# Performance work log

Measured on AMD Instinct MI355X. Metric: run time of the kernel, lower is better.

Reference implementation:

```python
import jax, jax.numpy as jnp
import numpy as np

DIM = 128
NUM_HEADS = 8


def setup_inputs() -> dict:
    key = jax.random.key(0)
    ks = jax.random.split(key, 5)
    B, L, C = 4, 16384, DIM
    x = jax.random.normal(ks[0], (B, L, C), dtype=jnp.float32)
    # Linear params (stored as (in, out) so y = x @ W + b)
    w_qkv = jax.random.normal(ks[1], (C, 3 * C), dtype=jnp.float32) * (C ** -0.5)
    b_qkv = jax.random.normal(ks[2], (3 * C,), dtype=jnp.float32) * 0.02
    w_proj = jax.random.normal(ks[3], (C, C), dtype=jnp.float32) * (C ** -0.5)
    b_proj = jax.random.normal(ks[4], (C,), dtype=jnp.float32) * 0.02
    return {"x": x, "w_qkv": w_qkv, "b_qkv": b_qkv, "w_proj": w_proj, "b_proj": b_proj}


def reference(x, w_qkv, b_qkv, w_proj, b_proj):
    B, L, C = x.shape
    H = NUM_HEADS
    hd = C // H
    scale = C ** -0.5  # note: torch code scales by dim**-0.5, not head_dim**-0.5

    qkv = x @ w_qkv + b_qkv                      # (B, L, 3C)
    q, k, v = jnp.split(qkv, 3, axis=-1)         # each (B, L, C)

    def to_heads(t):
        return t.reshape(B, L, H, hd).transpose(0, 2, 1, 3)  # (B, H, L, hd)

    q, k, v = to_heads(q), to_heads(k), to_heads(v)

    # Per-token outer product over head_dim: (B, H, L, hd, hd)
    attn = (q * scale)[..., :, None] * k[..., None, :]
    attn = jax.nn.softmax(attn, axis=-1)

    # attn @ v per token: (B, H, L, hd)
    out = jnp.einsum("bhlij,bhlj->bhli", attn, v)
    out = out.transpose(0, 2, 1, 3).reshape(B, L, C)  # (B, L, C)
    return out @ w_proj + b_proj
```

## Files before the change

### kernel.cpp

```cpp
#include <hip/hip_runtime.h>


typedef __attribute__((ext_vector_type(8))) short bf16x8;
typedef __attribute__((ext_vector_type(4))) float f32x4;
typedef __attribute__((ext_vector_type(4))) unsigned int u32x4;

#define TILE_M 32
#define HALF_M 16
#define QKV_STRIDE_F 388
#define O_STRIDE 136

__device__ __forceinline__ unsigned short f2bf(float f) {
    unsigned int u = __builtin_bit_cast(unsigned int, f);
    u += 0x8000u;
    return (unsigned short)(u >> 16);
}
__device__ __forceinline__ unsigned int pkbf(float lo, float hi) {
    unsigned int a = __builtin_bit_cast(unsigned int, lo) + 0x8000u;
    unsigned int b = __builtin_bit_cast(unsigned int, hi) + 0x8000u;
    return __builtin_amdgcn_perm(b, a, 0x07060302u);
}

__global__ void prep_weights(const float* __restrict__ wqkv,
                             const float* __restrict__ wproj,
                             unsigned short* __restrict__ wqkvT,
                             unsigned short* __restrict__ wprojT) {
    int idx = blockIdx.x * 256 + threadIdx.x;
    if (idx < 384 * 128) {
        int n = idx >> 7, k = idx & 127;
        wqkvT[idx] = f2bf(wqkv[k * 384 + n]);
    }
    if (idx < 128 * 128) {
        int n = idx >> 7, k = idx & 127;
        wprojT[idx] = f2bf(wproj[k * 128 + n]);
    }
}

__global__ __launch_bounds__(256, 4) void fused_channel_attn(
    const float* __restrict__ x,
    const unsigned short* __restrict__ wqkvT,
    const float* __restrict__ bqkv,
    const unsigned short* __restrict__ wprojT,
    const float* __restrict__ bproj,
    float* __restrict__ out)
{
    __shared__ __align__(16) float us_f[HALF_M * QKV_STRIDE_F];
    __shared__ __align__(16) unsigned short us_o[TILE_M * O_STRIDE];

    const int tid  = threadIdx.x;
    const int lane = tid & 63;
    const int wave = tid >> 6;
    const int col  = lane & 15;
    const int quad = lane >> 4;
    const long tok0 = (long)blockIdx.x * 2 * TILE_M;
    const long tok1 = tok0 + TILE_M;

    int ntile[6];
    ntile[0] = 2 * wave;      ntile[1] = 2 * wave + 1;
    ntile[2] = 8 + 2 * wave;  ntile[3] = 9 + 2 * wave;
    ntile[4] = 16 + 2 * wave; ntile[5] = 17 + 2 * wave;

    float bqv[6];
#pragma unroll
    for (int j = 0; j < 6; ++j) bqv[j] = bqkv[ntile[j] * 16 + col];

    bf16x8 afr[2][4];
    f32x4  acc[2][6];

    auto load_pack_x = [&](long bt) {
#pragma unroll
        for (int m = 0; m < 2; ++m) {
            const float* xrow = x + (bt + m * 16 + col) * 128;
#pragma unroll
            for (int ks = 0; ks < 4; ++ks) {
                const float4* p = (const float4*)(xrow + ks * 32 + quad * 8);
                float4 f0 = p[0], f1 = p[1];
                u32x4 a = {pkbf(f0.x, f0.y), pkbf(f0.z, f0.w),
                           pkbf(f1.x, f1.y), pkbf(f1.z, f1.w)};
                afr[m][ks] = __builtin_bit_cast(bf16x8, a);
            }
        }
    };

    auto mfma_qkv = [&]() {
#pragma unroll
        for (int j = 0; j < 6; ++j) {
            acc[0][j] = (f32x4){bqv[j], bqv[j], bqv[j], bqv[j]};
            acc[1][j] = (f32x4){bqv[j], bqv[j], bqv[j], bqv[j]};
        }
#pragma unroll
        for (int ks = 0; ks < 4; ++ks) {
            bf16x8 bfr[6];
#pragma unroll
            for (int j = 0; j < 6; ++j)
                bfr[j] = *(const bf16x8*)&wqkvT[(ntile[j] * 16 + col) * 128 + ks * 32 + quad * 8];
#pragma unroll
            for (int j = 0; j < 6; ++j) {
                acc[0][j] = __builtin_amdgcn_mfma_f32_16x16x32_bf16(afr[0][ks], bfr[j], acc[0][j], 0, 0, 0);
                acc[1][j] = __builtin_amdgcn_mfma_f32_16x16x32_bf16(afr[1][ks], bfr[j], acc[1][j], 0, 0, 0);
            }
        }
    };

    const int t    = lane & 15;
    const int hbit = (lane >> 4) & 1;
    const int ih   = lane >> 5;
    const int h    = 2 * wave + hbit;
    const float* qkvrow = us_f + t * QKV_STRIDE_F + h * 16;
    const float sl2e = 0.08838834764831845f * 1.44269504088896340f;

    auto write_half = [&](int m) {
#pragma unroll
        for (int j = 0; j < 6; ++j)
#pragma unroll
            for (int r = 0; r < 4; ++r)
                us_f[(quad * 4 + r) * QKV_STRIDE_F + ntile[j] * 16 + col] = acc[m][j][r];
    };

    float4 qv4[2], kv4[4], vv4[4];
    auto read_half = [&]() {
        qv4[0] = ((const float4*)(qkvrow + ih * 8))[0];
        qv4[1] = ((const float4*)(qkvrow + ih * 8))[1];
#pragma unroll
        for (int c = 0; c < 4; ++c) {
            kv4[c] = ((const float4*)(qkvrow + 128))[c];
            vv4[c] = ((const float4*)(qkvrow + 256))[c];
        }
    };

    auto attn_half = [&](int mhalf) {
        float qv[8], kf[16], vf[16];
#pragma unroll
        for (int c = 0; c < 2; ++c) {
            qv[4*c] = qv4[c].x; qv[4*c+1] = qv4[c].y; qv[4*c+2] = qv4[c].z; qv[4*c+3] = qv4[c].w;
        }
#pragma unroll
        for (int c = 0; c < 4; ++c) {
            kf[4*c] = kv4[c].x; kf[4*c+1] = kv4[c].y; kf[4*c+2] = kv4[c].z; kf[4*c+3] = kv4[c].w;
            vf[4*c] = vv4[c].x; vf[4*c+1] = vv4[c].y; vf[4*c+2] = vv4[c].z; vf[4*c+3] = vv4[c].w;
        }
        float ov[8];
#pragma unroll
        for (int i = 0; i < 8; ++i) {
            float qs = qv[i] * sl2e;
            float den = 0.f, num = 0.f;
#pragma unroll
            for (int j = 0; j < 16; ++j) {
                float e = __builtin_amdgcn_exp2f(qs * kf[j]);
                den += e;
                num = fmaf(e, vf[j], num);
            }
            ov[i] = num * __builtin_amdgcn_rcpf(den);
        }
        u32x4 o0 = {pkbf(ov[0], ov[1]), pkbf(ov[2], ov[3]),
                    pkbf(ov[4], ov[5]), pkbf(ov[6], ov[7])};
        *(u32x4*)&us_o[(mhalf * 16 + t) * O_STRIDE + h * 16 + ih * 8] = o0;
    };

    auto stage_c = [&](long bt) {
        const int nb2 = wave * 2;
#pragma unroll
        for (int m = 0; m < 2; ++m) {
            bf16x8 af[4];
#pragma unroll
            for (int ks = 0; ks < 4; ++ks)
                af[ks] = *(const bf16x8*)&us_o[(m * 16 + col) * O_STRIDE + ks * 32 + quad * 8];
            f32x4 acc2[2];
#pragma unroll
            for (int n = 0; n < 2; ++n) {
                float b = bproj[(nb2 + n) * 16 + col];
                acc2[n] = (f32x4){b, b, b, b};
            }
#pragma unroll
            for (int ks = 0; ks < 4; ++ks) {
                bf16x8 bb[2];
#pragma unroll
                for (int n = 0; n < 2; ++n)
                    bb[n] = *(const bf16x8*)&wprojT[((nb2 + n) * 16 + col) * 128 + ks * 32 + quad * 8];
#pragma unroll
                for (int n = 0; n < 2; ++n)
                    acc2[n] = __builtin_amdgcn_mfma_f32_16x16x32_bf16(af[ks], bb[n], acc2[n], 0, 0, 0);
            }
#pragma unroll
            for (int n = 0; n < 2; ++n)
#pragma unroll
                for (int r = 0; r < 4; ++r) {
                    long tt = bt + m * 16 + quad * 4 + r;
                    out[tt * 128 + (nb2 + n) * 16 + col] = acc2[n][r];
                }
        }
    };

    load_pack_x(tok0);
    mfma_qkv();

    write_half(0);
    read_half();

    float4 xp[8];
    {
        const float* xrow = x + (tok1 + col) * 128;
#pragma unroll
        for (int ks = 0; ks < 4; ++ks) {
            const float4* p = (const float4*)(xrow + ks * 32 + quad * 8);
            xp[2*ks] = p[0]; xp[2*ks+1] = p[1];
        }
    }
    write_half(1);
    attn_half(0);

#pragma unroll
    for (int ks = 0; ks < 4; ++ks) {
        float4 f0 = xp[2*ks], f1 = xp[2*ks+1];
        u32x4 a = {pkbf(f0.x, f0.y), pkbf(f0.z, f0.w),
                   pkbf(f1.x, f1.y), pkbf(f1.z, f1.w)};
        afr[0][ks] = __builtin_bit_cast(bf16x8, a);
    }
    {
        const float* xrow = x + (tok1 + 16 + col) * 128;
#pragma unroll
        for (int ks = 0; ks < 4; ++ks) {
            const float4* p = (const float4*)(xrow + ks * 32 + quad * 8);
            xp[2*ks] = p[0]; xp[2*ks+1] = p[1];
        }
    }
    read_half();
    attn_half(1);
#pragma unroll
    for (int ks = 0; ks < 4; ++ks) {
        float4 f0 = xp[2*ks], f1 = xp[2*ks+1];
        u32x4 a = {pkbf(f0.x, f0.y), pkbf(f0.z, f0.w),
                   pkbf(f1.x, f1.y), pkbf(f1.z, f1.w)};
        afr[1][ks] = __builtin_bit_cast(bf16x8, a);
    }

    __syncthreads();

    mfma_qkv();
    stage_c(tok0);

    __syncthreads();

    write_half(0);
    read_half();
    write_half(1);
    attn_half(0);
    read_half();
    attn_half(1);

    __syncthreads();
    stage_c(tok1);
}

extern "C" void kernel_launch(void* const* d_in, const int* in_sizes, int n_in,
                              void* d_out, int out_size, void* d_ws, size_t ws_size,
                              hipStream_t stream) {
    const float* x     = (const float*)d_in[0];
    const float* wqkv  = (const float*)d_in[1];
    const float* bqkv  = (const float*)d_in[2];
    const float* wproj = (const float*)d_in[3];
    const float* bproj = (const float*)d_in[4];
    float* out = (float*)d_out;

    unsigned short* wqkvT  = (unsigned short*)d_ws;
    unsigned short* wprojT = wqkvT + 384 * 128;

    prep_weights<<<192, 256, 0, stream>>>(wqkv, wproj, wqkvT, wprojT);

    const int tokens = in_sizes[0] / 128;
    fused_channel_attn<<<tokens / (2 * TILE_M), 256, 0, stream>>>(
        x, wqkvT, bqkv, wprojT, bproj, out);
}
```

Measured before the change: 139.6 us.

## Split fused kernel into QKV+attention and projection kernels via bf16 workspace

Breaks the single fused kernel into two launches: one computes QKV and the per-token channel attention, writing the bf16 attention output to a global workspace; the other runs the output projection. The goal is to free the first kernel from the us_o shared buffer and the projection registers so it can run with higher occupancy (launch bounds 5) and simpler scheduling, and to shrink each block to one 32-token tile. In exchange it adds an extra global write and read of a bf16 intermediate and a second launch, and falls back to a single-tile fused kernel when the workspace is too small.

```diff
diff --git a/kernel.cpp b/kernel.cpp
--- a/kernel.cpp
+++ b/kernel.cpp
@@ -36,7 +36,170 @@
     }
 }
 
-__global__ __launch_bounds__(256, 4) void fused_channel_attn(
+__global__ __launch_bounds__(256, 5) void qkv_attn(
+    const float* __restrict__ x,
+    const unsigned short* __restrict__ wqkvT,
+    const float* __restrict__ bqkv,
+    unsigned short* __restrict__ o)
+{
+    __shared__ __align__(16) float us_f[HALF_M * QKV_STRIDE_F];
+
+    const int tid  = threadIdx.x;
+    const int lane = tid & 63;
+    const int wave = tid >> 6;
+    const int col  = lane & 15;
+    const int quad = lane >> 4;
+    const long base_tok = (long)blockIdx.x * TILE_M;
+
+    int ntile[6];
+    ntile[0] = 2 * wave;      ntile[1] = 2 * wave + 1;
+    ntile[2] = 8 + 2 * wave;  ntile[3] = 9 + 2 * wave;
+    ntile[4] = 16 + 2 * wave; ntile[5] = 17 + 2 * wave;
+
+    f32x4 acc[2][6];
+#pragma unroll
+    for (int m = 0; m < 2; ++m) {
+        const float* xrow = x + (base_tok + m * 16 + col) * 128;
+        bf16x8 afr[4];
+#pragma unroll
+        for (int ks = 0; ks < 4; ++ks) {
+            const float4* p = (const float4*)(xrow + ks * 32 + quad * 8);
+            float4 f0 = p[0], f1 = p[1];
+            u32x4 a = {pkbf(f0.x, f0.y), pkbf(f0.z, f0.w),
+                       pkbf(f1.x, f1.y), pkbf(f1.z, f1.w)};
+            afr[ks] = __builtin_bit_cast(bf16x8, a);
+        }
+#pragma unroll
+        for (int j = 0; j < 6; ++j) {
+            float b = bqkv[ntile[j] * 16 + col];
+            acc[m][j] = (f32x4){b, b, b, b};
+        }
+#pragma unroll
+        for (int ks = 0; ks < 4; ++ks) {
+#pragma unroll
+            for (int jb = 0; jb < 2; ++jb) {
+                bf16x8 bfr[3];
+#pragma unroll
+                for (int j = 0; j < 3; ++j)
+                    bfr[j] = *(const bf16x8*)&wqkvT[(ntile[jb * 3 + j] * 16 + col) * 128 + ks * 32 + quad * 8];
+#pragma unroll
+                for (int j = 0; j < 3; ++j)
+                    acc[m][jb * 3 + j] = __builtin_amdgcn_mfma_f32_16x16x32_bf16(
+                        afr[ks], bfr[j], acc[m][jb * 3 + j], 0, 0, 0);
+            }
+        }
+    }
+
+    const int t    = lane & 15;
+    const int hbit = (lane >> 4) & 1;
+    const int ih   = lane >> 5;
+    const int h    = 2 * wave + hbit;
+    const float* qkvrow = us_f + t * QKV_STRIDE_F + h * 16;
+    const float sl2e = 0.08838834764831845f * 1.44269504088896340f;
+
+    auto write_half = [&](int m) {
+#pragma unroll
+        for (int j = 0; j < 6; ++j)
+#pragma unroll
+            for (int r = 0; r < 4; ++r)
+                us_f[(quad * 4 + r) * QKV_STRIDE_F + ntile[j] * 16 + col] = acc[m][j][r];
+    };
+
+    float4 qv4[2], kv4[4], vv4[4];
+    auto read_half = [&]() {
+        qv4[0] = ((const float4*)(qkvrow + ih * 8))[0];
+        qv4[1] = ((const float4*)(qkvrow + ih * 8))[1];
+#pragma unroll
+        for (int c = 0; c < 4; ++c) {
+            kv4[c] = ((const float4*)(qkvrow + 128))[c];
+            vv4[c] = ((const float4*)(qkvrow + 256))[c];
+        }
+    };
+
+    auto attn_half = [&](int mhalf) {
+        float qv[8], kf[16], vf[16];
+#pragma unroll
+        for (int c = 0; c < 2; ++c) {
+            qv[4*c] = qv4[c].x; qv[4*c+1] = qv4[c].y; qv[4*c+2] = qv4[c].z; qv[4*c+3] = qv4[c].w;
+        }
+#pragma unroll
+        for (int c = 0; c < 4; ++c) {
+            kf[4*c] = kv4[c].x; kf[4*c+1] = kv4[c].y; kf[4*c+2] = kv4[c].z; kf[4*c+3] = kv4[c].w;
+            vf[4*c] = vv4[c].x; vf[4*c+1] = vv4[c].y; vf[4*c+2] = vv4[c].z; vf[4*c+3] = vv4[c].w;
+        }
+        float ov[8];
+#pragma unroll
+        for (int i = 0; i < 8; ++i) {
+            float qs = qv[i] * sl2e;
+            float den = 0.f, num = 0.f;
+#pragma unroll
+            for (int j = 0; j < 16; ++j) {
+                float e = __builtin_amdgcn_exp2f(qs * kf[j]);
+                den += e;
+                num = fmaf(e, vf[j], num);
+            }
+            ov[i] = num * __builtin_amdgcn_rcpf(den);
+        }
+        u32x4 o0 = {pkbf(ov[0], ov[1]), pkbf(ov[2], ov[3]),
+                    pkbf(ov[4], ov[5]), pkbf(ov[6], ov[7])};
+        *(u32x4*)&o[(base_tok + mhalf * 16 + t) * 128 + h * 16 + ih * 8] = o0;
+    };
+
+    write_half(0);
+    read_half();
+    write_half(1);
+    attn_half(0);
+    read_half();
+    attn_half(1);
+}
+
+__global__ __launch_bounds__(256) void proj_out(
+    const unsigned short* __restrict__ o,
+    const unsigned short* __restrict__ wprojT,
+    const float* __restrict__ bproj,
+    float* __restrict__ out)
+{
+    const int tid  = threadIdx.x;
+    const int lane = tid & 63;
+    const int wave = tid >> 6;
+    const int col  = lane & 15;
+    const int quad = lane >> 4;
+    const long base_tok = (long)blockIdx.x * TILE_M;
+    const int nb2 = wave * 2;
+
+#pragma unroll
+    for (int m = 0; m < 2; ++m) {
+        bf16x8 af[4];
+#pragma unroll
+        for (int ks = 0; ks < 4; ++ks)
+            af[ks] = *(const bf16x8*)&o[(base_tok + m * 16 + col) * 128 + ks * 32 + quad * 8];
+        f32x4 acc2[2];
+#pragma unroll
+        for (int n = 0; n < 2; ++n) {
+            float b = bproj[(nb2 + n) * 16 + col];
+            acc2[n] = (f32x4){b, b, b, b};
+        }
+#pragma unroll
+        for (int ks = 0; ks < 4; ++ks) {
+            bf16x8 bb[2];
+#pragma unroll
+            for (int n = 0; n < 2; ++n)
+                bb[n] = *(const bf16x8*)&wprojT[((nb2 + n) * 16 + col) * 128 + ks * 32 + quad * 8];
+#pragma unroll
+            for (int n = 0; n < 2; ++n)
+                acc2[n] = __builtin_amdgcn_mfma_f32_16x16x32_bf16(af[ks], bb[n], acc2[n], 0, 0, 0);
+        }
+#pragma unroll
+        for (int n = 0; n < 2; ++n)
+#pragma unroll
+            for (int r = 0; r < 4; ++r) {
+                long tt = base_tok + m * 16 + quad * 4 + r;
+                out[tt * 128 + (nb2 + n) * 16 + col] = acc2[n][r];
+            }
+    }
+}
+
+__global__ __launch_bounds__(256, 4) void fused_channel_attn_fb(
     const float* __restrict__ x,
     const unsigned short* __restrict__ wqkvT,
     const float* __restrict__ bqkv,
@@ -52,55 +215,45 @@
     const int wave = tid >> 6;
     const int col  = lane & 15;
     const int quad = lane >> 4;
-    const long tok0 = (long)blockIdx.x * 2 * TILE_M;
-    const long tok1 = tok0 + TILE_M;
+    const long base_tok = (long)blockIdx.x * TILE_M;
 
     int ntile[6];
     ntile[0] = 2 * wave;      ntile[1] = 2 * wave + 1;
     ntile[2] = 8 + 2 * wave;  ntile[3] = 9 + 2 * wave;
     ntile[4] = 16 + 2 * wave; ntile[5] = 17 + 2 * wave;
 
-    float bqv[6];
-#pragma unroll
-    for (int j = 0; j < 6; ++j) bqv[j] = bqkv[ntile[j] * 16 + col];
-
     bf16x8 afr[2][4];
-    f32x4  acc[2][6];
-
-    auto load_pack_x = [&](long bt) {
-#pragma unroll
-        for (int m = 0; m < 2; ++m) {
-            const float* xrow = x + (bt + m * 16 + col) * 128;
-#pragma unroll
-            for (int ks = 0; ks < 4; ++ks) {
-                const float4* p = (const float4*)(xrow + ks * 32 + quad * 8);
-                float4 f0 = p[0], f1 = p[1];
-                u32x4 a = {pkbf(f0.x, f0.y), pkbf(f0.z, f0.w),
-                           pkbf(f1.x, f1.y), pkbf(f1.z, f1.w)};
-                afr[m][ks] = __builtin_bit_cast(bf16x8, a);
-            }
-        }
-    };
-
-    auto mfma_qkv = [&]() {
+#pragma unroll
+    for (int m = 0; m < 2; ++m) {
+        const float* xrow = x + (base_tok + m * 16 + col) * 128;
+#pragma unroll
+        for (int ks = 0; ks < 4; ++ks) {
+            const float4* p = (const float4*)(xrow + ks * 32 + quad * 8);
+            float4 f0 = p[0], f1 = p[1];
+            u32x4 a = {pkbf(f0.x, f0.y), pkbf(f0.z, f0.w),
+                       pkbf(f1.x, f1.y), pkbf(f1.z, f1.w)};
+            afr[m][ks] = __builtin_bit_cast(bf16x8, a);
+        }
+    }
+    f32x4 acc[2][6];
+#pragma unroll
+    for (int j = 0; j < 6; ++j) {
+        float b = bqkv[ntile[j] * 16 + col];
+        acc[0][j] = (f32x4){b, b, b, b};
+        acc[1][j] = (f32x4){b, b, b, b};
+    }
+#pragma unroll
+    for (int ks = 0; ks < 4; ++ks) {
+        bf16x8 bfr[6];
+#pragma unroll
+        for (int j = 0; j < 6; ++j)
+            bfr[j] = *(const bf16x8*)&wqkvT[(ntile[j] * 16 + col) * 128 + ks * 32 + quad * 8];
 #pragma unroll
         for (int j = 0; j < 6; ++j) {
-            acc[0][j] = (f32x4){bqv[j], bqv[j], bqv[j], bqv[j]};
-            acc[1][j] = (f32x4){bqv[j], bqv[j], bqv[j], bqv[j]};
-        }
-#pragma unroll
-        for (int ks = 0; ks < 4; ++ks) {
-            bf16x8 bfr[6];
-#pragma unroll
-            for (int j = 0; j < 6; ++j)
-                bfr[j] = *(const bf16x8*)&wqkvT[(ntile[j] * 16 + col) * 128 + ks * 32 + quad * 8];
-#pragma unroll
-            for (int j = 0; j < 6; ++j) {
-                acc[0][j] = __builtin_amdgcn_mfma_f32_16x16x32_bf16(afr[0][ks], bfr[j], acc[0][j], 0, 0, 0);
-                acc[1][j] = __builtin_amdgcn_mfma_f32_16x16x32_bf16(afr[1][ks], bfr[j], acc[1][j], 0, 0, 0);
-            }
-        }
-    };
+            acc[0][j] = __builtin_amdgcn_mfma_f32_16x16x32_bf16(afr[0][ks], bfr[j], acc[0][j], 0, 0, 0);
+            acc[1][j] = __builtin_amdgcn_mfma_f32_16x16x32_bf16(afr[1][ks], bfr[j], acc[1][j], 0, 0, 0);
+        }
+    }
 
     const int t    = lane & 15;
     const int hbit = (lane >> 4) & 1;
@@ -116,7 +269,6 @@
             for (int r = 0; r < 4; ++r)
                 us_f[(quad * 4 + r) * QKV_STRIDE_F + ntile[j] * 16 + col] = acc[m][j][r];
     };
-
     float4 qv4[2], kv4[4], vv4[4];
     auto read_half = [&]() {
         qv4[0] = ((const float4*)(qkvrow + ih * 8))[0];
@@ -127,7 +279,6 @@
             vv4[c] = ((const float4*)(qkvrow + 256))[c];
         }
     };
-
     auto attn_half = [&](int mhalf) {
         float qv[8], kf[16], vf[16];
 #pragma unroll
@@ -156,90 +307,6 @@
                     pkbf(ov[4], ov[5]), pkbf(ov[6], ov[7])};
         *(u32x4*)&us_o[(mhalf * 16 + t) * O_STRIDE + h * 16 + ih * 8] = o0;
     };
-
-    auto stage_c = [&](long bt) {
-        const int nb2 = wave * 2;
-#pragma unroll
-        for (int m = 0; m < 2; ++m) {
-            bf16x8 af[4];
-#pragma unroll
-            for (int ks = 0; ks < 4; ++ks)
-                af[ks] = *(const bf16x8*)&us_o[(m * 16 + col) * O_STRIDE + ks * 32 + quad * 8];
-            f32x4 acc2[2];
-#pragma unroll
-            for (int n = 0; n < 2; ++n) {
-                float b = bproj[(nb2 + n) * 16 + col];
-                acc2[n] = (f32x4){b, b, b, b};
-            }
-#pragma unroll
-            for (int ks = 0; ks < 4; ++ks) {
-                bf16x8 bb[2];
-#pragma unroll
-                for (int n = 0; n < 2; ++n)
-                    bb[n] = *(const bf16x8*)&wprojT[((nb2 + n) * 16 + col) * 128 + ks * 32 + quad * 8];
-#pragma unroll
-                for (int n = 0; n < 2; ++n)
-                    acc2[n] = __builtin_amdgcn_mfma_f32_16x16x32_bf16(af[ks], bb[n], acc2[n], 0, 0, 0);
-            }
-#pragma unroll
-            for (int n = 0; n < 2; ++n)
-#pragma unroll
-                for (int r = 0; r < 4; ++r) {
-                    long tt = bt + m * 16 + quad * 4 + r;
-                    out[tt * 128 + (nb2 + n) * 16 + col] = acc2[n][r];
-                }
-        }
-    };
-
-    load_pack_x(tok0);
-    mfma_qkv();
-
-    write_half(0);
-    read_half();
-
-    float4 xp[8];
-    {
-        const float* xrow = x + (tok1 + col) * 128;
-#pragma unroll
-        for (int ks = 0; ks < 4; ++ks) {
-            const float4* p = (const float4*)(xrow + ks * 32 + quad * 8);
-            xp[2*ks] = p[0]; xp[2*ks+1] = p[1];
-        }
-    }
-    write_half(1);
-    attn_half(0);
-
-#pragma unroll
-    for (int ks = 0; ks < 4; ++ks) {
-        float4 f0 = xp[2*ks], f1 = xp[2*ks+1];
-        u32x4 a = {pkbf(f0.x, f0.y), pkbf(f0.z, f0.w),
-                   pkbf(f1.x, f1.y), pkbf(f1.z, f1.w)};
-        afr[0][ks] = __builtin_bit_cast(bf16x8, a);
-    }
-    {
-        const float* xrow = x + (tok1 + 16 + col) * 128;
-#pragma unroll
-        for (int ks = 0; ks < 4; ++ks) {
-            const float4* p = (const float4*)(xrow + ks * 32 + quad * 8);
-            xp[2*ks] = p[0]; xp[2*ks+1] = p[1];
-        }
-    }
-    read_half();
-    attn_half(1);
-#pragma unroll
-    for (int ks = 0; ks < 4; ++ks) {
-        float4 f0 = xp[2*ks], f1 = xp[2*ks+1];
-        u32x4 a = {pkbf(f0.x, f0.y), pkbf(f0.z, f0.w),
-                   pkbf(f1.x, f1.y), pkbf(f1.z, f1.w)};
-        afr[1][ks] = __builtin_bit_cast(bf16x8, a);
-    }
-
-    __syncthreads();
-
-    mfma_qkv();
-    stage_c(tok0);
-
-    __syncthreads();
 
     write_half(0);
     read_half();
@@ -249,7 +316,38 @@
     attn_half(1);
 
     __syncthreads();
-    stage_c(tok1);
+
+    const int nb2 = wave * 2;
+#pragma unroll
+    for (int m = 0; m < 2; ++m) {
+        bf16x8 af[4];
+#pragma unroll
+        for (int ks = 0; ks < 4; ++ks)
+            af[ks] = *(const bf16x8*)&us_o[(m * 16 + col) * O_STRIDE + ks * 32 + quad * 8];
+        f32x4 acc2[2];
+#pragma unroll
+        for (int n = 0; n < 2; ++n) {
+            float b = bproj[(nb2 + n) * 16 + col];
+            acc2[n] = (f32x4){b, b, b, b};
+        }
+#pragma unroll
+        for (int ks = 0; ks < 4; ++ks) {
+            bf16x8 bb[2];
+#pragma unroll
+            for (int n = 0; n < 2; ++n)
+                bb[n] = *(const bf16x8*)&wprojT[((nb2 + n) * 16 + col) * 128 + ks * 32 + quad * 8];
+#pragma unroll
+            for (int n = 0; n < 2; ++n)
+                acc2[n] = __builtin_amdgcn_mfma_f32_16x16x32_bf16(af[ks], bb[n], acc2[n], 0, 0, 0);
+        }
+#pragma unroll
+        for (int n = 0; n < 2; ++n)
+#pragma unroll
+            for (int r = 0; r < 4; ++r) {
+                long tt = base_tok + m * 16 + quad * 4 + r;
+                out[tt * 128 + (nb2 + n) * 16 + col] = acc2[n][r];
+            }
+    }
 }
 
 extern "C" void kernel_launch(void* const* d_in, const int* in_sizes, int n_in,
@@ -264,10 +362,18 @@
 
     unsigned short* wqkvT  = (unsigned short*)d_ws;
     unsigned short* wprojT = wqkvT + 384 * 128;
+    unsigned short* o      = wprojT + 128 * 128;
 
     prep_weights<<<192, 256, 0, stream>>>(wqkv, wproj, wqkvT, wprojT);
 
     const int tokens = in_sizes[0] / 128;
-    fused_channel_attn<<<tokens / (2 * TILE_M), 256, 0, stream>>>(
-        x, wqkvT, bqkv, wprojT, bproj, out);
-}
+    const size_t ws_needed = (size_t)(384 + 128) * 128 * 2 + (size_t)tokens * 128 * 2;
+
+    if (ws_size >= ws_needed) {
+        qkv_attn<<<tokens / TILE_M, 256, 0, stream>>>(x, wqkvT, bqkv, o);
+        proj_out<<<tokens / TILE_M, 256, 0, stream>>>(o, wprojT, bproj, out);
+    } else {
+        fused_channel_attn_fb<<<tokens / TILE_M, 256, 0, stream>>>(
+            x, wqkvT, bqkv, wprojT, bproj, out);
+    }
+}
```

Measured after the change: 159.1 us. +14.0%, slower.
